# Optimization experiments

Hardware: AMD Instinct MI355X
Metric: run time of the kernel (lower is better)

The kernel has to match this reference:

```python
import jax, jax.numpy as jnp
import numpy as np

B, N, K, L, H = 8, 2048, 16, 4, 8
CONV = (64, 64, 128, 256)
W_DIM, N_CODES, E_DIM, P_DIM, FF = 512, 8, 64, 256, 512


def act(x):
    return jax.nn.leaky_relu(x, 0.2)


def ln(x, g, b, eps=1e-5):
    m = jnp.mean(x, -1, keepdims=True)
    v = jnp.mean((x - m) ** 2, -1, keepdims=True)
    return g * (x - m) / jnp.sqrt(v + eps) + b


# per-batch neighbor gather: f [C,N], i [N,K] -> [C,N,K]
gather_nb = jax.vmap(lambda f, i: f[:, i])


def knn_idx(y):  # y [B,3,N] -> [B,N,K]
    xx = jnp.sum(y * y, axis=1)
    inner = jnp.einsum('bcn,bcm->bnm', y, y)
    dist = 2.0 * inner - xx[:, :, None] - xx[:, None, :]  # negative sq dist
    return jax.lax.top_k(dist, K)[1]


def mha(q, kv, Wq, bq, Wk, bk, Wv, bv, Wo, bo):
    Bq, S, D = q.shape
    Sk = kv.shape[1]
    dh = D // H
    qh = (q @ Wq.T + bq).reshape(Bq, S, H, dh)
    kh = (kv @ Wk.T + bk).reshape(Bq, Sk, H, dh)
    vh = (kv @ Wv.T + bv).reshape(Bq, Sk, H, dh)
    a = jax.nn.softmax(jnp.einsum('bqhd,bkhd->bhqk', qh, kh) * (1.0 / np.sqrt(dh)))
    o = jnp.einsum('bhqk,bkhd->bqhd', a, vh).reshape(Bq, S, D)
    return o @ Wo.T + bo


def setup_inputs() -> dict:
    key = jax.random.key(0)
    ks = iter(jax.random.split(key, 48))
    nrm = lambda shape: jax.random.normal(next(ks), shape, jnp.float32) * 0.02
    d = {
        'x': jax.random.normal(next(ks), (B, N, 3), jnp.float32),
        'W_ec': nrm((CONV[0], 6)), 'b_ec': jnp.zeros((CONV[0],), jnp.float32),
        'Wc1': nrm((CONV[1], CONV[0])), 'bc1': jnp.zeros((CONV[1],), jnp.float32),
        'Wc2': nrm((CONV[2], CONV[1])), 'bc2': jnp.zeros((CONV[2],), jnp.float32),
        'Wc3': nrm((CONV[3], CONV[2])), 'bc3': jnp.zeros((CONV[3],), jnp.float32),
        'Wf': nrm((W_DIM, sum(CONV))), 'bf': jnp.zeros((W_DIM,), jnp.float32),
        'Wpc': nrm((P_DIM, E_DIM)), 'bpc': jnp.zeros((P_DIM,), jnp.float32),
        'Wpi': nrm((P_DIM, 3)), 'bpi': jnp.zeros((P_DIM,), jnp.float32),
        'Wq': nrm((L, 2, P_DIM, P_DIM)), 'bq': jnp.zeros((L, 2, P_DIM), jnp.float32),
        'Wk': nrm((L, 2, P_DIM, P_DIM)), 'bk': jnp.zeros((L, 2, P_DIM), jnp.float32),
        'Wv': nrm((L, 2, P_DIM, P_DIM)), 'bv': jnp.zeros((L, 2, P_DIM), jnp.float32),
        'Wo': nrm((L, 2, P_DIM, P_DIM)), 'bo': jnp.zeros((L, 2, P_DIM), jnp.float32),
        'ln1g': jnp.ones((L, P_DIM), jnp.float32), 'ln1b': jnp.zeros((L, P_DIM), jnp.float32),
        'ln2g': jnp.ones((L, P_DIM), jnp.float32), 'ln2b': jnp.zeros((L, P_DIM), jnp.float32),
        'Wff1': nrm((L, FF, P_DIM)), 'bff1': jnp.zeros((L, FF), jnp.float32),
        'Wff2': nrm((L, P_DIM, FF)), 'bff2': jnp.zeros((L, P_DIM), jnp.float32),
        'ln3g': jnp.ones((L, P_DIM), jnp.float32), 'ln3b': jnp.zeros((L, P_DIM), jnp.float32),
        'lnfg': jnp.ones((P_DIM,), jnp.float32), 'lnfb': jnp.zeros((P_DIM,), jnp.float32),
        'Wcm': nrm((E_DIM, P_DIM)), 'bcm': jnp.zeros((E_DIM,), jnp.float32),
    }
    return d


def reference(x, W_ec, b_ec, Wc1, bc1, Wc2, bc2, Wc3, bc3, Wf, bf, Wpc, bpc, Wpi, bpi,
              Wq, bq, Wk, bk, Wv, bv, Wo, bo, ln1g, ln1b, ln2g, ln2b,
              Wff1, bff1, Wff2, bff2, ln3g, ln3b, lnfg, lnfb, Wcm, bcm):
    y = jnp.transpose(x, (0, 2, 1))                      # [B,3,N]
    idx = knn_idx(y)                                     # [B,N,K]
    nb = gather_nb(y, idx)                               # [B,3,N,K]
    feats = jnp.concatenate([nb - y[..., None], jnp.broadcast_to(y[..., None], nb.shape)], axis=1)
    h = act(jnp.einsum('oc,bcnk->bonk', W_ec, feats) + b_ec[:, None, None])
    h = h.max(axis=3)                                    # [B,64,N]
    xs = [h]
    for Wl, bl in ((Wc1, bc1), (Wc2, bc2), (Wc3, bc3)):
        h = gather_nb(h, idx).max(axis=3)                # graph max pooling
        h = act(jnp.einsum('oc,bcn->bon', Wl, h) + bl[:, None])
        xs.append(h)
    h = jnp.concatenate(xs, axis=1)                      # [B,512,N]
    h = jnp.einsum('oc,bcn->bon', Wf, h) + bf[:, None]
    xm = h.max(axis=2)                                   # [B,512]
    q = act(xm.reshape(B, N_CODES, E_DIM) @ Wpc.T + bpc) # [B,8,256]
    mem = act(x @ Wpi.T + bpi)                           # [B,N,256]
    for l in range(L):
        q = ln(q + mha(q, q, Wq[l, 0], bq[l, 0], Wk[l, 0], bk[l, 0], Wv[l, 0], bv[l, 0], Wo[l, 0], bo[l, 0]), ln1g[l], ln1b[l])
        q = ln(q + mha(q, mem, Wq[l, 1], bq[l, 1], Wk[l, 1], bk[l, 1], Wv[l, 1], bv[l, 1], Wo[l, 1], bo[l, 1]), ln2g[l], ln2b[l])
        q = ln(q + (act(q @ Wff1[l].T + bff1[l]) @ Wff2[l].T + bff2[l]), ln3g[l], ln3b[l])
    q = ln(q, lnfg, lnfb)
    out = q @ Wcm.T + bcm                                # [B,8,64]
    return out.reshape(B, W_DIM)
```

## Files before the change

### kernel.cpp

```cpp
#include <hip/hip_runtime.h>
#include <math.h>

#define BN 8
#define NP 2048
#define KNN 16
#define NL 4
#define NH 8

typedef __attribute__((ext_vector_type(8))) short bf16x8;
typedef __attribute__((ext_vector_type(4))) float f32x4;

__device__ __forceinline__ unsigned short f2bf(float f) {
    unsigned u = __float_as_uint(f);
    unsigned r = (u + 0x7FFFu + ((u >> 16) & 1u)) >> 16;
    return (unsigned short)r;
}
__device__ __forceinline__ float bf2f(unsigned short s) {
    return __uint_as_float(((unsigned)s) << 16);
}
__device__ __forceinline__ unsigned fmono(float f) {
    unsigned u = __float_as_uint(f);
    return (u & 0x80000000u) ? ~u : (u | 0x80000000u);
}
__device__ __forceinline__ float funmono(unsigned k) {
    return (k & 0x80000000u) ? __uint_as_float(k ^ 0x80000000u) : __uint_as_float(~k);
}

__device__ __forceinline__ float gemv_dot(const unsigned short* __restrict__ wrow, const float* sm, int K8) {
    const uint4* w8 = (const uint4*)wrow;
    const float4* r4 = (const float4*)sm;
    float acc = 0.f;
    #pragma unroll 16
    for (int c = 0; c < K8; ++c) {
        uint4 wv = w8[c];
        float4 a0 = r4[c * 2], a1 = r4[c * 2 + 1];
        acc += a0.x * __uint_as_float(wv.x << 16);
        acc += a0.y * __uint_as_float(wv.x & 0xFFFF0000u);
        acc += a0.z * __uint_as_float(wv.y << 16);
        acc += a0.w * __uint_as_float(wv.y & 0xFFFF0000u);
        acc += a1.x * __uint_as_float(wv.z << 16);
        acc += a1.y * __uint_as_float(wv.z & 0xFFFF0000u);
        acc += a1.z * __uint_as_float(wv.w << 16);
        acc += a1.w * __uint_as_float(wv.w & 0xFFFF0000u);
    }
    return acc;
}

__device__ __forceinline__ unsigned long long shflx_u64(unsigned long long v, int j) {
    int lo = __shfl_xor((int)(unsigned)(v & 0xFFFFFFFFull), j);
    int hi = __shfl_xor((int)(unsigned)(v >> 32), j);
    return ((unsigned long long)(unsigned)hi << 32) | (unsigned)lo;
}

__device__ __forceinline__ unsigned sort64_u32(unsigned v, int lane) {
    #pragma unroll
    for (int k = 2; k <= 64; k <<= 1) {
        #pragma unroll
        for (int j = k >> 1; j > 0; j >>= 1) {
            unsigned o = (unsigned)__shfl_xor((int)v, j);
            bool up = ((lane & k) == 0);
            bool lower = ((lane & j) == 0);
            unsigned mn = v < o ? v : o;
            unsigned mx = v < o ? o : v;
            v = (up == lower) ? mn : mx;
        }
    }
    return v;
}

__device__ __forceinline__ unsigned long long sort64_u64(unsigned long long v, int lane) {
    #pragma unroll
    for (int k = 2; k <= 64; k <<= 1) {
        #pragma unroll
        for (int j = k >> 1; j > 0; j >>= 1) {
            unsigned long long o = shflx_u64(v, j);
            bool up = ((lane & k) == 0);
            bool lower = ((lane & j) == 0);
            unsigned long long mn = v < o ? v : o;
            unsigned long long mx = v < o ? o : v;
            v = (up == lower) ? mn : mx;
        }
    }
    return v;
}

__global__ __launch_bounds__(256) void knn_kernel(const float* __restrict__ x, int* __restrict__ idxout) {
    __shared__ unsigned long long cand[4][64];
    int tid = threadIdx.x;
    int wv = tid >> 6, lane = tid & 63;
    int p = blockIdx.x * 4 + wv;
    int b = p >> 11, n = p & 2047;
    const float* xb = x + (size_t)b * NP * 3;
    float cx = xb[n * 3 + 0], cy = xb[n * 3 + 1], cz = xb[n * 3 + 2];
    float xn = cx * cx + cy * cy + cz * cz;
    unsigned key[32];
    unsigned lmax = 0u;
    #pragma unroll
    for (int t = 0; t < 32; ++t) {
        int m = (t << 6) | lane;
        float mx = xb[m * 3 + 0], my = xb[m * 3 + 1], mz = xb[m * 3 + 2];
        float xxm = mx * mx + my * my + mz * mz;
        float inner = cx * mx + cy * my + cz * mz;
        float dd = 2.0f * inner - xn - xxm;
        unsigned u = __float_as_uint(dd);
        u = (u & 0x80000000u) ? ~u : (u | 0x80000000u);
        key[t] = u;
        lmax = lmax > u ? lmax : u;
    }
    unsigned sorted = sort64_u32(lmax, lane);
    unsigned S = (unsigned)__shfl((int)sorted, 48);
    int c = 0;
    #pragma unroll
    for (int t = 0; t < 32; ++t) c += (key[t] >= S) ? 1 : 0;
    int inc = c;
    #pragma unroll
    for (int d = 1; d < 64; d <<= 1) {
        int tsh = __shfl_up(inc, d);
        if (lane >= d) inc += tsh;
    }
    int C = __shfl(inc, 63);
    int* op = idxout + (size_t)p * KNN;
    if (C <= 64) {
        int off = inc - c;
        #pragma unroll
        for (int t = 0; t < 32; ++t) {
            if (key[t] >= S) {
                int m = (t << 6) | lane;
                cand[wv][off++] = ((unsigned long long)key[t] << 16) | (unsigned)(2047 - m);
            }
        }
        asm volatile("s_waitcnt lgkmcnt(0)" ::: "memory");
        unsigned long long ck = (lane < C) ? cand[wv][lane] : 0ull;
        ck = sort64_u64(ck, lane);
        if (lane >= 48) op[63 - lane] = 2047 - (int)(unsigned)(ck & 0xFFFFull);
    } else {
        unsigned taken = 0u;
        for (int r = 0; r < KNN; ++r) {
            unsigned long long best = 0ull;
            #pragma unroll
            for (int t = 0; t < 32; ++t) {
                if (!((taken >> t) & 1u)) {
                    int m = (t << 6) | lane;
                    unsigned long long ck = ((unsigned long long)key[t] << 16) | (unsigned)(2047 - m);
                    if (ck > best) best = ck;
                }
            }
            #pragma unroll
            for (int d = 1; d < 64; d <<= 1) {
                unsigned long long o = shflx_u64(best, d);
                if (o > best) best = o;
            }
            int m = 2047 - (int)(unsigned)(best & 0xFFFFull);
            if (lane == 0) op[r] = m;
            if ((m & 63) == lane) taken |= 1u << (m >> 6);
        }
    }
}

__global__ __launch_bounds__(256) void edge_conv_kernel(const float* __restrict__ x, const int* __restrict__ idx,
                                                        const float* __restrict__ Wec, const float* __restrict__ bec,
                                                        unsigned short* __restrict__ hcatT) {
    int tid = threadIdx.x;
    int g = tid >> 6, o = tid & 63;
    int p = blockIdx.x * 4 + g;
    int b = p >> 11;
    __shared__ float nb[4][KNN][3];
    __shared__ float ctr[4][3];
    if (o < KNN) {
        int j = idx[(size_t)p * KNN + o];
        const float* xp = x + ((size_t)b * NP + j) * 3;
        nb[g][o][0] = xp[0]; nb[g][o][1] = xp[1]; nb[g][o][2] = xp[2];
    }
    if (o >= KNN && o < KNN + 3) ctr[g][o - KNN] = x[(size_t)p * 3 + (o - KNN)];
    __syncthreads();
    float w0 = Wec[o * 6 + 0], w1 = Wec[o * 6 + 1], w2 = Wec[o * 6 + 2];
    float w3 = Wec[o * 6 + 3], w4 = Wec[o * 6 + 4], w5 = Wec[o * 6 + 5];
    float c0 = ctr[g][0], c1 = ctr[g][1], c2 = ctr[g][2];
    float base = bec[o] + w3 * c0 + w4 * c1 + w5 * c2;
    float m = -3.4e38f;
    #pragma unroll
    for (int k = 0; k < KNN; ++k) {
        float v = base + w0 * (nb[g][k][0] - c0) + w1 * (nb[g][k][1] - c1) + w2 * (nb[g][k][2] - c2);
        v = v > 0.f ? v : 0.2f * v;
        m = fmaxf(m, v);
    }
    hcatT[(size_t)p * 512 + o] = f2bf(m);
}

__global__ __launch_bounds__(256) void pool_bf16_kernel(const unsigned short* __restrict__ src, int s_coff,
                                                        const int* __restrict__ idx,
                                                        unsigned short* __restrict__ dst, int C) {
    int tid = threadIdx.x, wv = tid >> 6, lane = tid & 63;
    int p = blockIdx.x * 4 + wv;
    int b = p >> 11;
    const int* ip = idx + (size_t)p * KNN;
    const unsigned short* sb = src + (size_t)b * NP * 512 + s_coff;
    for (int c0 = 0; c0 < C; c0 += 64) {
        int ch = c0 + lane;
        float m = -3.4e38f;
        #pragma unroll
        for (int k = 0; k < KNN; ++k) {
            int j = ip[k];
            m = fmaxf(m, bf2f(sb[(size_t)j * 512 + ch]));
        }
        dst[(size_t)p * C + ch] = f2bf(m);
    }
}

__global__ __launch_bounds__(256) void mfma_conv64_kernel(const unsigned short* __restrict__ A,
                                                          const unsigned short* __restrict__ W,
                                                          const float* __restrict__ bias,
                                                          unsigned short* __restrict__ hcatT, int coff) {
    __shared__ unsigned short As[128][72];
    __shared__ unsigned short Bs[64][72];
    int m0 = blockIdx.x * 128, b = blockIdx.z;
    int tid = threadIdx.x;
    int lane = tid & 63, wave = tid >> 6;
    int wr = wave >> 1, wc = wave & 1;
    int quad = lane >> 4, l16 = lane & 15;
    {
        int r = tid >> 1, s = (tid & 1) * 32;
        const unsigned short* ap = A + (size_t)b * NP * 64 + (size_t)(m0 + r) * 64 + s;
        uint4 v0 = *(const uint4*)(ap);
        uint4 v1 = *(const uint4*)(ap + 8);
        uint4 v2 = *(const uint4*)(ap + 16);
        uint4 v3 = *(const uint4*)(ap + 24);
        *(uint4*)&As[r][s] = v0; *(uint4*)&As[r][s + 8] = v1;
        *(uint4*)&As[r][s + 16] = v2; *(uint4*)&As[r][s + 24] = v3;
    }
    {
        int r = tid >> 2, s = (tid & 3) * 16;
        const unsigned short* wp = W + r * 64 + s;
        *(uint4*)&Bs[r][s] = *(const uint4*)wp;
        *(uint4*)&Bs[r][s + 8] = *(const uint4*)(wp + 8);
    }
    __syncthreads();
    f32x4 acc[4][2] = {};
    #pragma unroll
    for (int k0 = 0; k0 < 64; k0 += 32) {
        bf16x8 af[4], bfv[2];
        #pragma unroll
        for (int i = 0; i < 4; ++i) af[i] = *(const bf16x8*)&As[wr * 64 + i * 16 + l16][k0 + quad * 8];
        #pragma unroll
        for (int j = 0; j < 2; ++j) bfv[j] = *(const bf16x8*)&Bs[wc * 32 + j * 16 + l16][k0 + quad * 8];
        #pragma unroll
        for (int i = 0; i < 4; ++i)
            #pragma unroll
            for (int j = 0; j < 2; ++j)
                acc[i][j] = __builtin_amdgcn_mfma_f32_16x16x32_bf16(af[i], bfv[j], acc[i][j], 0, 0, 0);
    }
    #pragma unroll
    for (int i = 0; i < 4; ++i) {
        #pragma unroll
        for (int r = 0; r < 4; ++r) {
            int pt = m0 + wr * 64 + i * 16 + quad * 4 + r;
            #pragma unroll
            for (int j = 0; j < 2; ++j) {
                int ch = wc * 32 + j * 16 + l16;
                float v = acc[i][j][r] + bias[ch];
                v = v > 0.f ? v : 0.2f * v;
                hcatT[((size_t)b * NP + pt) * 512 + coff + ch] = f2bf(v);
            }
        }
    }
}

__global__ __launch_bounds__(256) void wcast_kernel(const float* __restrict__ Wf, const float* __restrict__ Wc3,
                                                    const float* __restrict__ Wk, const float* __restrict__ Wv,
                                                    const float* __restrict__ bk, const float* __restrict__ bv,
                                                    const float* __restrict__ Wc1, const float* __restrict__ Wc2,
                                                    const float* __restrict__ Wq, const float* __restrict__ Wo,
                                                    const float* __restrict__ Wff1, const float* __restrict__ Wff2,
                                                    unsigned short* __restrict__ WfB, unsigned short* __restrict__ Wc3B,
                                                    unsigned short* __restrict__ WkvB, float* __restrict__ bkv,
                                                    unsigned short* __restrict__ Wc1B, unsigned short* __restrict__ Wc2B,
                                                    unsigned short* __restrict__ WtB, unsigned short* __restrict__ Wff1B,
                                                    unsigned short* __restrict__ Wff2B,
                                                    unsigned* __restrict__ xmk) {
    int id = blockIdx.x * 256 + threadIdx.x;
    if (id < 262144) { WfB[id] = f2bf(Wf[id]); return; }
    int j = id - 262144;
    if (j < 32768) { Wc3B[j] = f2bf(Wc3[j]); return; }
    j -= 32768;
    if (j < 524288) {
        int l = j >> 17, r = j & 131071;
        float v = (r < 65536) ? Wk[(size_t)(l * 2 + 1) * 65536 + r]
                              : Wv[(size_t)(l * 2 + 1) * 65536 + (r - 65536)];
        WkvB[j] = f2bf(v);
        return;
    }
    j -= 524288;
    if (j < 2048) {
        int l = j >> 9, r = j & 511;
        bkv[j] = (r < 256) ? bk[(l * 2 + 1) * 256 + r] : bv[(l * 2 + 1) * 256 + (r - 256)];
        return;
    }
    j -= 2048;
    if (j < 4096) { Wc1B[j] = f2bf(Wc1[j]); return; }
    j -= 4096;
    if (j < 8192) { Wc2B[j] = f2bf(Wc2[j]); return; }
    j -= 8192;
    if (j < 4096) { xmk[j] = 0u; return; }
    j -= 4096;
    if (j < 1572864) {
        int l = j / 393216;
        int r = j - l * 393216;
        int m = r >> 16, c = r & 65535;
        float v;
        if (m == 0)      v = Wq[(size_t)(l * 2 + 0) * 65536 + c];
        else if (m == 1) v = Wk[(size_t)(l * 2 + 0) * 65536 + c];
        else if (m == 2) v = Wv[(size_t)(l * 2 + 0) * 65536 + c];
        else if (m == 3) v = Wo[(size_t)(l * 2 + 0) * 65536 + c];
        else if (m == 4) v = Wq[(size_t)(l * 2 + 1) * 65536 + c];
        else             v = Wo[(size_t)(l * 2 + 1) * 65536 + c];
        WtB[j] = f2bf(v);
        return;
    }
    j -= 1572864;
    if (j < 524288) { Wff1B[j] = f2bf(Wff1[j]); return; }
    j -= 524288;
    if (j < 524288) { Wff2B[j] = f2bf(Wff2[j]); return; }
}

__global__ __launch_bounds__(256) void mfma_gemm_kernel(const unsigned short* __restrict__ A, size_t a_bstride,
                                                        const unsigned short* __restrict__ B, size_t b_bstride,
                                                        const float* __restrict__ bias, int bias_per_m,
                                                        void* __restrict__ C, size_t c_bstride, int c_rstride,
                                                        int K, int act, int out_bf16,
                                                        unsigned* __restrict__ xmk, int domax) {
    __shared__ unsigned short As[128][40];
    __shared__ unsigned short Bs[128][40];
    int m0 = blockIdx.x * 128, n0 = blockIdx.y * 128, b = blockIdx.z;
    int tid = threadIdx.x;
    int lane = tid & 63, wave = tid >> 6;
    int wr = wave >> 1, wc = wave & 1;
    int quad = lane >> 4, l16 = lane & 15;
    int r0 = tid >> 2, kc0 = (tid & 3) * 8;
    f32x4 acc[4][4] = {};
    const unsigned short* Ab = A + (size_t)b * a_bstride;
    const unsigned short* Bb = B + (size_t)b * b_bstride;
    for (int k0 = 0; k0 < K; k0 += 32) {
        uint4 a0 = *(const uint4*)(Ab + (size_t)(m0 + r0) * K + k0 + kc0);
        uint4 a1 = *(const uint4*)(Ab + (size_t)(m0 + r0 + 64) * K + k0 + kc0);
        uint4 b0 = *(const uint4*)(Bb + (size_t)(n0 + r0) * K + k0 + kc0);
        uint4 b1 = *(const uint4*)(Bb + (size_t)(n0 + r0 + 64) * K + k0 + kc0);
        __syncthreads();
        *(uint4*)&As[r0][kc0] = a0;
        *(uint4*)&As[r0 + 64][kc0] = a1;
        *(uint4*)&Bs[r0][kc0] = b0;
        *(uint4*)&Bs[r0 + 64][kc0] = b1;
        __syncthreads();
        bf16x8 af[4], bfv[4];
        #pragma unroll
        for (int i = 0; i < 4; ++i) af[i] = *(const bf16x8*)&As[wr * 64 + i * 16 + l16][quad * 8];
        #pragma unroll
        for (int j = 0; j < 4; ++j) bfv[j] = *(const bf16x8*)&Bs[wc * 64 + j * 16 + l16][quad * 8];
        #pragma unroll
        for (int i = 0; i < 4; ++i)
            #pragma unroll
            for (int j = 0; j < 4; ++j)
                acc[i][j] = __builtin_amdgcn_mfma_f32_16x16x32_bf16(af[i], bfv[j], acc[i][j], 0, 0, 0);
    }
    if (domax) {
        #pragma unroll
        for (int i = 0; i < 4; ++i) {
            #pragma unroll
            for (int r = 0; r < 4; ++r) {
                int m = m0 + wr * 64 + i * 16 + quad * 4 + r;
                float v = fmaxf(fmaxf(acc[i][0][r], acc[i][1][r]), fmaxf(acc[i][2][r], acc[i][3][r]));
                v += bias[m];
                #pragma unroll
                for (int off = 1; off <= 8; off <<= 1) v = fmaxf(v, __shfl_xor(v, off));
                if (l16 == 0) atomicMax(&xmk[(size_t)b * 512 + m], fmono(v));
            }
        }
        return;
    }
    #pragma unroll
    for (int i = 0; i < 4; ++i) {
        #pragma unroll
        for (int r = 0; r < 4; ++r) {
            int m = m0 + wr * 64 + i * 16 + quad * 4 + r;
            float bm = bias_per_m ? bias[m] : 0.f;
            #pragma unroll
            for (int j = 0; j < 4; ++j) {
                int n = n0 + wc * 64 + j * 16 + l16;
                float v = acc[i][j][r] + (bias_per_m ? bm : bias[n]);
                if (act) v = v > 0.f ? v : 0.2f * v;
                size_t off = (size_t)b * c_bstride + (size_t)m * c_rstride + n;
                if (out_bf16) ((unsigned short*)C)[off] = f2bf(v);
                else          ((float*)C)[off] = v;
            }
        }
    }
}

__global__ __launch_bounds__(256) void mfma_kv_all_kernel(const unsigned short* __restrict__ A,
                                                          const unsigned short* __restrict__ W,
                                                          const float* __restrict__ bkv,
                                                          unsigned short* __restrict__ KVall) {
    __shared__ unsigned short As[128][40];
    __shared__ unsigned short Bs[128][40];
    int m0 = blockIdx.x * 128;
    int nb = blockIdx.y & 3, l = blockIdx.y >> 2;
    int n0 = nb * 128;
    int b = blockIdx.z;
    int tid = threadIdx.x;
    int lane = tid & 63, wave = tid >> 6;
    int wr = wave >> 1, wc = wave & 1;
    int quad = lane >> 4, l16 = lane & 15;
    int r0 = tid >> 2, kc0 = (tid & 3) * 8;
    f32x4 acc[4][4] = {};
    const unsigned short* Ab = A + (size_t)b * NP * 256;
    const unsigned short* Bb = W + (size_t)l * 131072;
    const float* bias = bkv + l * 512;
    for (int k0 = 0; k0 < 256; k0 += 32) {
        uint4 a0 = *(const uint4*)(Ab + (size_t)(m0 + r0) * 256 + k0 + kc0);
        uint4 a1 = *(const uint4*)(Ab + (size_t)(m0 + r0 + 64) * 256 + k0 + kc0);
        uint4 b0 = *(const uint4*)(Bb + (size_t)(n0 + r0) * 256 + k0 + kc0);
        uint4 b1 = *(const uint4*)(Bb + (size_t)(n0 + r0 + 64) * 256 + k0 + kc0);
        __syncthreads();
        *(uint4*)&As[r0][kc0] = a0;
        *(uint4*)&As[r0 + 64][kc0] = a1;
        *(uint4*)&Bs[r0][kc0] = b0;
        *(uint4*)&Bs[r0 + 64][kc0] = b1;
        __syncthreads();
        bf16x8 af[4], bfv[4];
        #pragma unroll
        for (int i = 0; i < 4; ++i) af[i] = *(const bf16x8*)&As[wr * 64 + i * 16 + l16][quad * 8];
        #pragma unroll
        for (int j = 0; j < 4; ++j) bfv[j] = *(const bf16x8*)&Bs[wc * 64 + j * 16 + l16][quad * 8];
        #pragma unroll
        for (int i = 0; i < 4; ++i)
            #pragma unroll
            for (int j = 0; j < 4; ++j)
                acc[i][j] = __builtin_amdgcn_mfma_f32_16x16x32_bf16(af[i], bfv[j], acc[i][j], 0, 0, 0);
    }
    unsigned short* Cb = KVall + ((size_t)l * BN + b) * NP * 512;
    #pragma unroll
    for (int i = 0; i < 4; ++i) {
        #pragma unroll
        for (int r = 0; r < 4; ++r) {
            int m = m0 + wr * 64 + i * 16 + quad * 4 + r;
            #pragma unroll
            for (int j = 0; j < 4; ++j) {
                int n = n0 + wc * 64 + j * 16 + l16;
                Cb[(size_t)m * 512 + n] = f2bf(acc[i][j][r] + bias[n]);
            }
        }
    }
}

__global__ __launch_bounds__(256) void pc_kernel(const unsigned* __restrict__ xmk, const float* __restrict__ Wpc,
                                                 const float* __restrict__ bpc,
                                                 const unsigned short* __restrict__ Wqkv,
                                                 const float* __restrict__ bq0, const float* __restrict__ bk0,
                                                 const float* __restrict__ bv0,
                                                 float* __restrict__ q, float* __restrict__ Qs,
                                                 float* __restrict__ Ks, float* __restrict__ Vs) {
    int row = blockIdx.x, tid = threadIdx.x;
    int id = row * 256 + tid;
    int b = row >> 3, i = row & 7;
    const unsigned* xr = xmk + b * 512 + i * 64;
    const float* w = Wpc + (size_t)tid * 64;
    float acc = bpc[tid];
    #pragma unroll
    for (int e = 0; e < 64; ++e) acc += funmono(xr[e]) * w[e];
    float qv = acc > 0.f ? acc : 0.2f * acc;
    q[id] = qv;
    __shared__ __align__(16) float a[256];
    a[tid] = qv;
    __syncthreads();
    Qs[id] = bq0[tid] + gemv_dot(Wqkv + (size_t)tid * 256, a, 32);
    Ks[id] = bk0[tid] + gemv_dot(Wqkv + 65536 + (size_t)tid * 256, a, 32);
    Vs[id] = bv0[tid] + gemv_dot(Wqkv + 131072 + (size_t)tid * 256, a, 32);
}

__global__ __launch_bounds__(256) void mem_kernel(const float* __restrict__ x, const float* __restrict__ Wpi,
                                                  const float* __restrict__ bpi, unsigned short* __restrict__ memB) {
    size_t id = (size_t)blockIdx.x * 256 + threadIdx.x;
    int p = (int)(id & 255);
    size_t pt = id >> 8;
    float x0 = x[pt * 3 + 0], x1 = x[pt * 3 + 1], x2 = x[pt * 3 + 2];
    float v = bpi[p] + x0 * Wpi[p * 3 + 0] + x1 * Wpi[p * 3 + 1] + x2 * Wpi[p * 3 + 2];
    v = v > 0.f ? v : 0.2f * v;
    memB[id] = f2bf(v);
}

__global__ __launch_bounds__(256) void attn_ln_kernel(const float* __restrict__ Qs, const float* __restrict__ Ks,
                                                      const float* __restrict__ Vs,
                                                      const unsigned short* __restrict__ WoB,
                                                      const float* __restrict__ bo, const float* __restrict__ res,
                                                      const float* __restrict__ g, const float* __restrict__ bt,
                                                      const unsigned short* __restrict__ Wq1B,
                                                      const float* __restrict__ bq1,
                                                      float* __restrict__ out, float* __restrict__ Qc) {
    int row = blockIdx.x, tid = threadIdx.x;
    int b = row >> 3;
    __shared__ float Kl[2048], Vl[2048], qr[256];
    __shared__ float sc[64];
    __shared__ __align__(16) float r[256];
    __shared__ __align__(16) float aout[256];
    __shared__ float red[256];
    for (int t = tid; t < 2048; t += 256) {
        Kl[t] = Ks[(size_t)b * 2048 + t];
        Vl[t] = Vs[(size_t)b * 2048 + t];
    }
    qr[tid] = Qs[(size_t)row * 256 + tid];
    __syncthreads();
    const float scale = 0.17677669529663687f;
    {
        int pair = tid >> 2, part = tid & 3;
        int h = pair >> 3, k = pair & 7;
        float dot = 0.f;
        #pragma unroll
        for (int d0 = 0; d0 < 8; ++d0) {
            int d = part * 8 + d0;
            dot += qr[h * 32 + d] * Kl[k * 256 + h * 32 + d];
        }
        dot += __shfl_xor(dot, 1);
        dot += __shfl_xor(dot, 2);
        if (part == 0) sc[pair] = dot * scale;
    }
    __syncthreads();
    if (tid < 64) {
        int k = tid & 7;
        float v = sc[tid];
        float m = v;
        #pragma unroll
        for (int off = 1; off < 8; off <<= 1) m = fmaxf(m, __shfl_xor(m, off));
        float e = __expf(v - m);
        float s = e;
        #pragma unroll
        for (int off = 1; off < 8; off <<= 1) s += __shfl_xor(s, off);
        sc[tid] = e / s;
        (void)k;
    }
    __syncthreads();
    {
        int h = tid >> 5;
        float acc = 0.f;
        #pragma unroll
        for (int k = 0; k < 8; ++k) acc += sc[h * 8 + k] * Vl[k * 256 + tid];
        r[tid] = acc;
    }
    __syncthreads();
    float acc = bo[tid] + gemv_dot(WoB + (size_t)tid * 256, r, 32);
    float v = res[(size_t)row * 256 + tid] + acc;
    red[tid] = v; __syncthreads();
    for (int s = 128; s; s >>= 1) { if (tid < s) red[tid] += red[tid + s]; __syncthreads(); }
    float mean = red[0] * (1.0f / 256.0f);
    __syncthreads();
    float dv = v - mean;
    red[tid] = dv * dv; __syncthreads();
    for (int s = 128; s; s >>= 1) { if (tid < s) red[tid] += red[tid + s]; __syncthreads(); }
    float var = red[0] * (1.0f / 256.0f);
    float oln = g[tid] * dv * rsqrtf(var + 1e-5f) + bt[tid];
    out[(size_t)row * 256 + tid] = oln;
    aout[tid] = oln;
    __syncthreads();
    {
        float qacc = bq1[tid] + gemv_dot(Wq1B + (size_t)tid * 256, aout, 32);
        Qc[(size_t)row * 256 + tid] = qacc;
    }
}

__global__ __launch_bounds__(256) void ca_part_kernel(const float* __restrict__ Qc,
                                                      const unsigned short* __restrict__ KVl,
                                                      float* __restrict__ part) {
    int kb = blockIdx.x, h = blockIdx.y, b = blockIdx.z;
    int tid = threadIdx.x;
    __shared__ float q[8][32];
    __shared__ __align__(16) float S[8][128];
    __shared__ float om[8][8][32];
    const float scale = 0.17677669529663687f;
    {
        int i = tid >> 5, d = tid & 31;
        q[i][d] = Qc[(size_t)(b * 8 + i) * 256 + h * 32 + d];
    }
    __syncthreads();
    {
        int kk = tid & 127, half = tid >> 7;
        int k = kb * 128 + kk;
        const unsigned short* kp = KVl + ((size_t)b * NP + k) * 512 + h * 32;
        float kd[32];
        #pragma unroll
        for (int u = 0; u < 4; ++u) {
            uint4 raw = *(const uint4*)(kp + u * 8);
            unsigned w0 = raw.x, w1 = raw.y, w2 = raw.z, w3 = raw.w;
            kd[u * 8 + 0] = __uint_as_float(w0 << 16); kd[u * 8 + 1] = __uint_as_float(w0 & 0xFFFF0000u);
            kd[u * 8 + 2] = __uint_as_float(w1 << 16); kd[u * 8 + 3] = __uint_as_float(w1 & 0xFFFF0000u);
            kd[u * 8 + 4] = __uint_as_float(w2 << 16); kd[u * 8 + 5] = __uint_as_float(w2 & 0xFFFF0000u);
            kd[u * 8 + 6] = __uint_as_float(w3 << 16); kd[u * 8 + 7] = __uint_as_float(w3 & 0xFFFF0000u);
        }
        #pragma unroll
        for (int i = 0; i < 4; ++i) {
            int ri = half * 4 + i;
            float dot = 0.f;
            #pragma unroll
            for (int d = 0; d < 32; ++d) dot += q[ri][d] * kd[d];
            S[ri][kk] = dot * scale;
        }
    }
    __syncthreads();
    float* pout = part + (((size_t)(b * NH + h)) * 16 + kb) * 288;
    {
        int i = tid >> 5, l32 = tid & 31;
        float m = -3.4e38f;
        #pragma unroll
        for (int t = 0; t < 4; ++t) m = fmaxf(m, S[i][l32 + t * 32]);
        #pragma unroll
        for (int off = 16; off; off >>= 1) m = fmaxf(m, __shfl_xor(m, off));
        float s = 0.f;
        #pragma unroll
        for (int t = 0; t < 4; ++t) {
            float e = __expf(S[i][l32 + t * 32] - m);
            S[i][l32 + t * 32] = e;
            s += e;
        }
        #pragma unroll
        for (int off = 16; off; off >>= 1) s += __shfl_xor(s, off);
        if (l32 == 0) { pout[i] = m; pout[8 + i] = s; }
    }
    __syncthreads();
    {
        int d = tid & 31, grp = tid >> 5;
        const unsigned short* Vb = KVl + ((size_t)b * NP + kb * 128) * 512 + 256 + h * 32 + d;
        float acc[8] = {};
        #pragma unroll 4
        for (int t = 0; t < 16; ++t) {
            int kk = grp * 16 + t;
            float v = bf2f(Vb[(size_t)kk * 512]);
            #pragma unroll
            for (int i = 0; i < 8; ++i) acc[i] += S[i][kk] * v;
        }
        #pragma unroll
        for (int i = 0; i < 8; ++i) om[grp][i][d] = acc[i];
    }
    __syncthreads();
    {
        int i = tid >> 5, d = tid & 31;
        float sum = 0.f;
        #pragma unroll
        for (int g = 0; g < 8; ++g) sum += om[g][i][d];
        pout[16 + i * 32 + d] = sum;
    }
}

__global__ __launch_bounds__(256) void combine_ff_kernel(const float* __restrict__ part,
                                                         const unsigned short* __restrict__ WoB,
                                                         const float* __restrict__ bo, const float* __restrict__ res,
                                                         const float* __restrict__ g2, const float* __restrict__ b2t,
                                                         const unsigned short* __restrict__ W1B,
                                                         const float* __restrict__ b1,
                                                         const unsigned short* __restrict__ W2B,
                                                         const float* __restrict__ b2,
                                                         const float* __restrict__ g3, const float* __restrict__ b3t,
                                                         float* __restrict__ out,
                                                         int is_last, const float* __restrict__ lnfg,
                                                         const float* __restrict__ lnfb, const float* __restrict__ Wcm,
                                                         const float* __restrict__ bcm, float* __restrict__ finout,
                                                         const unsigned short* __restrict__ Wqkvn,
                                                         const float* __restrict__ bqn, const float* __restrict__ bkn,
                                                         const float* __restrict__ bvn,
                                                         float* __restrict__ Qs, float* __restrict__ Ks,
                                                         float* __restrict__ Vs) {
    int row = blockIdx.x, tid = threadIdx.x;
    int b = row >> 3, i = row & 7;
    __shared__ __align__(16) float r[256];
    __shared__ __align__(16) float a[256];
    __shared__ __align__(16) float hbuf[512];
    __shared__ float red[256];
    {
        int h = tid >> 5, d = tid & 31;
        const float* pb = part + (size_t)(b * NH + h) * 16 * 288;
        float M = -3.4e38f;
        #pragma unroll
        for (int kb = 0; kb < 16; ++kb) M = fmaxf(M, pb[kb * 288 + i]);
        float L = 0.f, O = 0.f;
        #pragma unroll
        for (int kb = 0; kb < 16; ++kb) {
            float w = __expf(pb[kb * 288 + i] - M);
            L += pb[kb * 288 + 8 + i] * w;
            O += pb[kb * 288 + 16 + i * 32 + d] * w;
        }
        r[tid] = O / L;
    }
    __syncthreads();
    {
        float acc = bo[tid] + gemv_dot(WoB + (size_t)tid * 256, r, 32);
        float v = res[(size_t)row * 256 + tid] + acc;
        red[tid] = v; __syncthreads();
        for (int s = 128; s; s >>= 1) { if (tid < s) red[tid] += red[tid + s]; __syncthreads(); }
        float mean = red[0] * (1.0f / 256.0f);
        __syncthreads();
        float dv = v - mean;
        red[tid] = dv * dv; __syncthreads();
        for (int s = 128; s; s >>= 1) { if (tid < s) red[tid] += red[tid + s]; __syncthreads(); }
        float var = red[0] * (1.0f / 256.0f);
        a[tid] = g2[tid] * dv * rsqrtf(var + 1e-5f) + b2t[tid];
    }
    __syncthreads();
    {
        #pragma unroll
        for (int half = 0; half < 2; ++half) {
            int o = tid + half * 256;
            float acc = b1[o] + gemv_dot(W1B + (size_t)o * 256, a, 32);
            hbuf[o] = acc > 0.f ? acc : 0.2f * acc;
        }
    }
    __syncthreads();
    float tln;
    {
        float acc = b2[tid] + gemv_dot(W2B + (size_t)tid * 512, hbuf, 64);
        float v = a[tid] + acc;
        red[tid] = v; __syncthreads();
        for (int s = 128; s; s >>= 1) { if (tid < s) red[tid] += red[tid + s]; __syncthreads(); }
        float mean = red[0] * (1.0f / 256.0f);
        __syncthreads();
        float dv = v - mean;
        red[tid] = dv * dv; __syncthreads();
        for (int s = 128; s; s >>= 1) { if (tid < s) red[tid] += red[tid + s]; __syncthreads(); }
        float var = red[0] * (1.0f / 256.0f);
        tln = g3[tid] * dv * rsqrtf(var + 1e-5f) + b3t[tid];
    }
    if (!is_last) {
        out[(size_t)row * 256 + tid] = tln;
        r[tid] = tln;
        __syncthreads();
        size_t id = (size_t)row * 256 + tid;
        Qs[id] = bqn[tid] + gemv_dot(Wqkvn + (size_t)tid * 256, r, 32);
        Ks[id] = bkn[tid] + gemv_dot(Wqkvn + 65536 + (size_t)tid * 256, r, 32);
        Vs[id] = bvn[tid] + gemv_dot(Wqkvn + 131072 + (size_t)tid * 256, r, 32);
        return;
    }
    __syncthreads();
    red[tid] = tln; __syncthreads();
    for (int s = 128; s; s >>= 1) { if (tid < s) red[tid] += red[tid + s]; __syncthreads(); }
    float mean = red[0] * (1.0f / 256.0f);
    __syncthreads();
    float dv = tln - mean;
    red[tid] = dv * dv; __syncthreads();
    for (int s = 128; s; s >>= 1) { if (tid < s) red[tid] += red[tid + s]; __syncthreads(); }
    float var = red[0] * (1.0f / 256.0f);
    a[tid] = lnfg[tid] * dv * rsqrtf(var + 1e-5f) + lnfb[tid];
    __syncthreads();
    if (tid < 64) {
        const float4* w4 = (const float4*)(Wcm + (size_t)tid * 256);
        const float4* a4 = (const float4*)a;
        float acc = bcm[tid];
        #pragma unroll 8
        for (int c = 0; c < 64; ++c) {
            float4 av = a4[c], wv = w4[c];
            acc += av.x * wv.x + av.y * wv.y + av.z * wv.z + av.w * wv.w;
        }
        finout[(size_t)b * 512 + i * 64 + tid] = acc;
    }
}

extern "C" void kernel_launch(void* const* d_in, const int* in_sizes, int n_in,
                              void* d_out, int out_size, void* d_ws, size_t ws_size,
                              hipStream_t stream) {
    const float* x    = (const float*)d_in[0];
    const float* Wec  = (const float*)d_in[1];
    const float* bec  = (const float*)d_in[2];
    const float* Wc1  = (const float*)d_in[3];
    const float* bc1  = (const float*)d_in[4];
    const float* Wc2  = (const float*)d_in[5];
    const float* bc2  = (const float*)d_in[6];
    const float* Wc3  = (const float*)d_in[7];
    const float* bc3  = (const float*)d_in[8];
    const float* Wf   = (const float*)d_in[9];
    const float* bf   = (const float*)d_in[10];
    const float* Wpc  = (const float*)d_in[11];
    const float* bpc  = (const float*)d_in[12];
    const float* Wpi  = (const float*)d_in[13];
    const float* bpi  = (const float*)d_in[14];
    const float* Wq   = (const float*)d_in[15];
    const float* bq   = (const float*)d_in[16];
    const float* Wk   = (const float*)d_in[17];
    const float* bk   = (const float*)d_in[18];
    const float* Wv   = (const float*)d_in[19];
    const float* bv   = (const float*)d_in[20];
    const float* Wo   = (const float*)d_in[21];
    const float* bo   = (const float*)d_in[22];
    const float* ln1g = (const float*)d_in[23];
    const float* ln1b = (const float*)d_in[24];
    const float* ln2g = (const float*)d_in[25];
    const float* ln2b = (const float*)d_in[26];
    const float* Wff1 = (const float*)d_in[27];
    const float* bff1 = (const float*)d_in[28];
    const float* Wff2 = (const float*)d_in[29];
    const float* bff2 = (const float*)d_in[30];
    const float* ln3g = (const float*)d_in[31];
    const float* ln3b = (const float*)d_in[32];
    const float* lnfg = (const float*)d_in[33];
    const float* lnfb = (const float*)d_in[34];
    const float* Wcm  = (const float*)d_in[35];
    const float* bcm  = (const float*)d_in[36];
    float* out = (float*)d_out;

    float* ws = (float*)d_ws;
    size_t off = 0;
    auto alloc = [&](size_t n) { float* p = ws + off; off += (n + 3) & ~(size_t)3; return p; };
    int*            idx   = (int*)alloc((size_t)BN * NP * KNN);
    unsigned short* hcatT = (unsigned short*)alloc((size_t)BN * NP * 512 / 2);
    unsigned short* poolT = (unsigned short*)alloc((size_t)BN * NP * 128 / 2);
    unsigned short* WfB   = (unsigned short*)alloc(262144 / 2);
    unsigned short* Wc1B  = (unsigned short*)alloc(4096 / 2);
    unsigned short* Wc2B  = (unsigned short*)alloc(8192 / 2);
    unsigned short* Wc3B  = (unsigned short*)alloc(32768 / 2);
    unsigned short* WkvB  = (unsigned short*)alloc(524288 / 2);
    float*          bkv   = alloc(2048);
    unsigned short* memB  = (unsigned short*)alloc((size_t)BN * NP * 256 / 2);
    unsigned short* KVall = (unsigned short*)alloc((size_t)NL * BN * NP * 512 / 2);
    unsigned*       xmk   = (unsigned*)alloc((size_t)BN * 512);
    unsigned short* WtB   = (unsigned short*)alloc(1572864 / 2);
    unsigned short* Wff1B = (unsigned short*)alloc(524288 / 2);
    unsigned short* Wff2B = (unsigned short*)alloc(524288 / 2);
    float*          qa    = alloc((size_t)BN * 8 * 256);
    float*          qb    = alloc((size_t)BN * 8 * 256);
    float*          Qs    = alloc((size_t)BN * 8 * 256);
    float*          Ks    = alloc((size_t)BN * 8 * 256);
    float*          Vs    = alloc((size_t)BN * 8 * 256);
    float*          Qc    = alloc((size_t)BN * 8 * 256);
    float*          part  = alloc((size_t)BN * NH * 16 * 288);

    wcast_kernel<<<13512, 256, 0, stream>>>(Wf, Wc3, Wk, Wv, bk, bv, Wc1, Wc2, Wq, Wo, Wff1, Wff2,
                                            WfB, Wc3B, WkvB, bkv, Wc1B, Wc2B, WtB, Wff1B, Wff2B, xmk);

    knn_kernel<<<BN * NP / 4, 256, 0, stream>>>(x, idx);
    edge_conv_kernel<<<BN * NP / 4, 256, 0, stream>>>(x, idx, Wec, bec, hcatT);

    pool_bf16_kernel<<<BN * NP / 4, 256, 0, stream>>>(hcatT, 0, idx, poolT, 64);
    mfma_conv64_kernel<<<dim3(NP / 128, 1, BN), 256, 0, stream>>>(poolT, Wc1B, bc1, hcatT, 64);
    pool_bf16_kernel<<<BN * NP / 4, 256, 0, stream>>>(hcatT, 64, idx, poolT, 64);
    mfma_gemm_kernel<<<dim3(NP / 128, 1, BN), 256, 0, stream>>>(poolT, (size_t)NP * 64, Wc2B, 0,
                                                                bc2, 0, (void*)(hcatT + 128), (size_t)NP * 512, 512,
                                                                64, 1, 1, nullptr, 0);
    pool_bf16_kernel<<<BN * NP / 4, 256, 0, stream>>>(hcatT, 128, idx, poolT, 128);
    mfma_gemm_kernel<<<dim3(NP / 128, 2, BN), 256, 0, stream>>>(poolT, (size_t)NP * 128, Wc3B, 0,
                                                                bc3, 0, (void*)(hcatT + 256), (size_t)NP * 512, 512,
                                                                128, 1, 1, nullptr, 0);
    mfma_gemm_kernel<<<dim3(4, NP / 128, BN), 256, 0, stream>>>(WfB, 0, hcatT, (size_t)NP * 512,
                                                                bf, 1, nullptr, 0, 0,
                                                                512, 0, 0, xmk, 1);
    pc_kernel<<<BN * 8, 256, 0, stream>>>(xmk, Wpc, bpc, WtB, bq, bk, bv, qa, Qs, Ks, Vs);
    mem_kernel<<<BN * NP, 256, 0, stream>>>(x, Wpi, bpi, memB);
    mfma_kv_all_kernel<<<dim3(NP / 128, 4 * NL, BN), 256, 0, stream>>>(memB, WkvB, bkv, KVall);

    for (int l = 0; l < NL; ++l) {
        const unsigned short* Wl = WtB + (size_t)l * 393216;
        const float* bo0 = bo + (l * 2 + 0) * 256;
        const float* bq1 = bq + (l * 2 + 1) * 256;
        const float* bo1 = bo + (l * 2 + 1) * 256;
        int last = (l == NL - 1);

        attn_ln_kernel<<<BN * 8, 256, 0, stream>>>(Qs, Ks, Vs, Wl + 3 * 65536, bo0, qa,
                                                   ln1g + l * 256, ln1b + l * 256, Wl + 4 * 65536, bq1, qb, Qc);
        ca_part_kernel<<<dim3(16, NH, BN), 256, 0, stream>>>(Qc, KVall + (size_t)l * BN * NP * 512, part);
        combine_ff_kernel<<<BN * 8, 256, 0, stream>>>(part, Wl + 5 * 65536, bo1, qb,
                                                      ln2g + l * 256, ln2b + l * 256,
                                                      Wff1B + (size_t)l * 131072, bff1 + l * 512,
                                                      Wff2B + (size_t)l * 131072, bff2 + l * 256,
                                                      ln3g + l * 256, ln3b + l * 256, qa,
                                                      last, lnfg, lnfb, Wcm, bcm, out,
                                                      last ? nullptr : WtB + (size_t)(l + 1) * 393216,
                                                      bq + ((l + 1) * 2) * 256, bk + ((l + 1) * 2) * 256,
                                                      bv + ((l + 1) * 2) * 256,
                                                      Qs, Ks, Vs);
    }

    (void)in_sizes; (void)n_in; (void)out_size; (void)ws_size;
}
```

Before: 591.7 us.

## Split GEMV rows across four threads in 1024-thread decoder blocks

```diff
diff --git a/kernel.cpp b/kernel.cpp
--- a/kernel.cpp
+++ b/kernel.cpp
@@ -29,21 +29,17 @@
 __device__ __forceinline__ float gemv_dot(const unsigned short* __restrict__ wrow, const float* sm, int K8) {
     const uint4* w8 = (const uint4*)wrow;
     const float4* r4 = (const float4*)sm;
-    float acc = 0.f;
-    #pragma unroll 16
+    float a0 = 0.f, a1 = 0.f, a2 = 0.f, a3 = 0.f;
+    #pragma unroll 8
     for (int c = 0; c < K8; ++c) {
         uint4 wv = w8[c];
-        float4 a0 = r4[c * 2], a1 = r4[c * 2 + 1];
-        acc += a0.x * __uint_as_float(wv.x << 16);
-        acc += a0.y * __uint_as_float(wv.x & 0xFFFF0000u);
-        acc += a0.z * __uint_as_float(wv.y << 16);
-        acc += a0.w * __uint_as_float(wv.y & 0xFFFF0000u);
-        acc += a1.x * __uint_as_float(wv.z << 16);
-        acc += a1.y * __uint_as_float(wv.z & 0xFFFF0000u);
-        acc += a1.z * __uint_as_float(wv.w << 16);
-        acc += a1.w * __uint_as_float(wv.w & 0xFFFF0000u);
-    }
-    return acc;
+        float4 x0 = r4[c * 2], x1 = r4[c * 2 + 1];
+        a0 += x0.x * __uint_as_float(wv.x << 16) + x0.y * __uint_as_float(wv.x & 0xFFFF0000u);
+        a1 += x0.z * __uint_as_float(wv.y << 16) + x0.w * __uint_as_float(wv.y & 0xFFFF0000u);
+        a2 += x1.x * __uint_as_float(wv.z << 16) + x1.y * __uint_as_float(wv.z & 0xFFFF0000u);
+        a3 += x1.z * __uint_as_float(wv.w << 16) + x1.w * __uint_as_float(wv.w & 0xFFFF0000u);
+    }
+    return (a0 + a1) + (a2 + a3);
 }
 
 __device__ __forceinline__ unsigned long long shflx_u64(unsigned long long v, int j) {
@@ -487,44 +483,43 @@
     memB[id] = f2bf(v);
 }
 
-__global__ __launch_bounds__(256) void attn_ln_kernel(const float* __restrict__ Qs, const float* __restrict__ Ks,
-                                                      const float* __restrict__ Vs,
-                                                      const unsigned short* __restrict__ WoB,
-                                                      const float* __restrict__ bo, const float* __restrict__ res,
-                                                      const float* __restrict__ g, const float* __restrict__ bt,
-                                                      const unsigned short* __restrict__ Wq1B,
-                                                      const float* __restrict__ bq1,
-                                                      float* __restrict__ out, float* __restrict__ Qc) {
+__global__ __launch_bounds__(1024) void attn_ln_kernel(const float* __restrict__ Qs, const float* __restrict__ Ks,
+                                                       const float* __restrict__ Vs,
+                                                       const unsigned short* __restrict__ WoB,
+                                                       const float* __restrict__ bo, const float* __restrict__ res,
+                                                       const float* __restrict__ g, const float* __restrict__ bt,
+                                                       const unsigned short* __restrict__ Wq1B,
+                                                       const float* __restrict__ bq1,
+                                                       float* __restrict__ out, float* __restrict__ Qc) {
     int row = blockIdx.x, tid = threadIdx.x;
     int b = row >> 3;
-    __shared__ float Kl[2048], Vl[2048], qr[256];
+    __shared__ float Kl[2048], Vl[2048];
+    __shared__ __align__(16) float qr[256];
     __shared__ float sc[64];
     __shared__ __align__(16) float r[256];
     __shared__ __align__(16) float aout[256];
-    __shared__ float red[256];
-    for (int t = tid; t < 2048; t += 256) {
+    __shared__ float red[1024];
+    for (int t = tid; t < 2048; t += 1024) {
         Kl[t] = Ks[(size_t)b * 2048 + t];
         Vl[t] = Vs[(size_t)b * 2048 + t];
     }
-    qr[tid] = Qs[(size_t)row * 256 + tid];
+    if (tid < 256) qr[tid] = Qs[(size_t)row * 256 + tid];
     __syncthreads();
     const float scale = 0.17677669529663687f;
     {
-        int pair = tid >> 2, part = tid & 3;
+        int pair = tid >> 4, part = tid & 15;
         int h = pair >> 3, k = pair & 7;
-        float dot = 0.f;
-        #pragma unroll
-        for (int d0 = 0; d0 < 8; ++d0) {
-            int d = part * 8 + d0;
-            dot += qr[h * 32 + d] * Kl[k * 256 + h * 32 + d];
-        }
+        int d = part * 2;
+        float dot = qr[h * 32 + d] * Kl[k * 256 + h * 32 + d]
+                  + qr[h * 32 + d + 1] * Kl[k * 256 + h * 32 + d + 1];
         dot += __shfl_xor(dot, 1);
         dot += __shfl_xor(dot, 2);
+        dot += __shfl_xor(dot, 4);
+        dot += __shfl_xor(dot, 8);
         if (part == 0) sc[pair] = dot * scale;
     }
     __syncthreads();
     if (tid < 64) {
-        int k = tid & 7;
         float v = sc[tid];
         float m = v;
         #pragma unroll
@@ -534,10 +529,9 @@
         #pragma unroll
         for (int off = 1; off < 8; off <<= 1) s += __shfl_xor(s, off);
         sc[tid] = e / s;
-        (void)k;
-    }
-    __syncthreads();
-    {
+    }
+    __syncthreads();
+    if (tid < 256) {
         int h = tid >> 5;
         float acc = 0.f;
         #pragma unroll
@@ -545,23 +539,33 @@
         r[tid] = acc;
     }
     __syncthreads();
-    float acc = bo[tid] + gemv_dot(WoB + (size_t)tid * 256, r, 32);
-    float v = res[(size_t)row * 256 + tid] + acc;
+    int o4 = tid >> 2, p4 = tid & 3;
+    float v;
+    {
+        float acc = gemv_dot(WoB + (size_t)o4 * 256 + p4 * 64, r + p4 * 64, 8);
+        acc += __shfl_xor(acc, 1);
+        acc += __shfl_xor(acc, 2);
+        v = (p4 == 0) ? (bo[o4] + acc + res[(size_t)row * 256 + o4]) : 0.f;
+    }
     red[tid] = v; __syncthreads();
-    for (int s = 128; s; s >>= 1) { if (tid < s) red[tid] += red[tid + s]; __syncthreads(); }
+    for (int s = 512; s; s >>= 1) { if (tid < s) red[tid] += red[tid + s]; __syncthreads(); }
     float mean = red[0] * (1.0f / 256.0f);
     __syncthreads();
-    float dv = v - mean;
+    float dv = (p4 == 0) ? v - mean : 0.f;
     red[tid] = dv * dv; __syncthreads();
-    for (int s = 128; s; s >>= 1) { if (tid < s) red[tid] += red[tid + s]; __syncthreads(); }
+    for (int s = 512; s; s >>= 1) { if (tid < s) red[tid] += red[tid + s]; __syncthreads(); }
     float var = red[0] * (1.0f / 256.0f);
-    float oln = g[tid] * dv * rsqrtf(var + 1e-5f) + bt[tid];
-    out[(size_t)row * 256 + tid] = oln;
-    aout[tid] = oln;
-    __syncthreads();
-    {
-        float qacc = bq1[tid] + gemv_dot(Wq1B + (size_t)tid * 256, aout, 32);
-        Qc[(size_t)row * 256 + tid] = qacc;
+    if (p4 == 0) {
+        float oln = g[o4] * dv * rsqrtf(var + 1e-5f) + bt[o4];
+        out[(size_t)row * 256 + o4] = oln;
+        aout[o4] = oln;
+    }
+    __syncthreads();
+    {
+        float qacc = gemv_dot(Wq1B + (size_t)o4 * 256 + p4 * 64, aout + p4 * 64, 8);
+        qacc += __shfl_xor(qacc, 1);
+        qacc += __shfl_xor(qacc, 2);
+        if (p4 == 0) Qc[(size_t)row * 256 + o4] = bq1[o4] + qacc;
     }
 }
 
@@ -647,103 +651,118 @@
     }
 }
 
-__global__ __launch_bounds__(256) void combine_ff_kernel(const float* __restrict__ part,
-                                                         const unsigned short* __restrict__ WoB,
-                                                         const float* __restrict__ bo, const float* __restrict__ res,
-                                                         const float* __restrict__ g2, const float* __restrict__ b2t,
-                                                         const unsigned short* __restrict__ W1B,
-                                                         const float* __restrict__ b1,
-                                                         const unsigned short* __restrict__ W2B,
-                                                         const float* __restrict__ b2,
-                                                         const float* __restrict__ g3, const float* __restrict__ b3t,
-                                                         float* __restrict__ out,
-                                                         int is_last, const float* __restrict__ lnfg,
-                                                         const float* __restrict__ lnfb, const float* __restrict__ Wcm,
-                                                         const float* __restrict__ bcm, float* __restrict__ finout,
-                                                         const unsigned short* __restrict__ Wqkvn,
-                                                         const float* __restrict__ bqn, const float* __restrict__ bkn,
-                                                         const float* __restrict__ bvn,
-                                                         float* __restrict__ Qs, float* __restrict__ Ks,
-                                                         float* __restrict__ Vs) {
+__global__ __launch_bounds__(1024) void combine_ff_kernel(const float* __restrict__ part,
+                                                          const unsigned short* __restrict__ WoB,
+                                                          const float* __restrict__ bo, const float* __restrict__ res,
+                                                          const float* __restrict__ g2, const float* __restrict__ b2t,
+                                                          const unsigned short* __restrict__ W1B,
+                                                          const float* __restrict__ b1,
+                                                          const unsigned short* __restrict__ W2B,
+                                                          const float* __restrict__ b2,
+                                                          const float* __restrict__ g3, const float* __restrict__ b3t,
+                                                          float* __restrict__ out,
+                                                          int is_last, const float* __restrict__ lnfg,
+                                                          const float* __restrict__ lnfb, const float* __restrict__ Wcm,
+                                                          const float* __restrict__ bcm, float* __restrict__ finout,
+                                                          const unsigned short* __restrict__ Wqkvn,
+                                                          const float* __restrict__ bqn, const float* __restrict__ bkn,
+                                                          const float* __restrict__ bvn,
+                                                          float* __restrict__ Qs, float* __restrict__ Ks,
+                                                          float* __restrict__ Vs) {
     int row = blockIdx.x, tid = threadIdx.x;
     int b = row >> 3, i = row & 7;
     __shared__ __align__(16) float r[256];
     __shared__ __align__(16) float a[256];
     __shared__ __align__(16) float hbuf[512];
-    __shared__ float red[256];
-    {
-        int h = tid >> 5, d = tid & 31;
+    __shared__ float red[1024];
+    {
+        int h = tid >> 7, rem = tid & 127, d = rem >> 2, g = rem & 3;
         const float* pb = part + (size_t)(b * NH + h) * 16 * 288;
         float M = -3.4e38f;
         #pragma unroll
-        for (int kb = 0; kb < 16; ++kb) M = fmaxf(M, pb[kb * 288 + i]);
+        for (int t = 0; t < 4; ++t) M = fmaxf(M, pb[(g * 4 + t) * 288 + i]);
+        M = fmaxf(M, __shfl_xor(M, 1));
+        M = fmaxf(M, __shfl_xor(M, 2));
         float L = 0.f, O = 0.f;
         #pragma unroll
-        for (int kb = 0; kb < 16; ++kb) {
+        for (int t = 0; t < 4; ++t) {
+            int kb = g * 4 + t;
             float w = __expf(pb[kb * 288 + i] - M);
             L += pb[kb * 288 + 8 + i] * w;
             O += pb[kb * 288 + 16 + i * 32 + d] * w;
         }
-        r[tid] = O / L;
-    }
-    __syncthreads();
-    {
-        float acc = bo[tid] + gemv_dot(WoB + (size_t)tid * 256, r, 32);
-        float v = res[(size_t)row * 256 + tid] + acc;
-        red[tid] = v; __syncthreads();
-        for (int s = 128; s; s >>= 1) { if (tid < s) red[tid] += red[tid + s]; __syncthreads(); }
-        float mean = red[0] * (1.0f / 256.0f);
-        __syncthreads();
-        float dv = v - mean;
-        red[tid] = dv * dv; __syncthreads();
-        for (int s = 128; s; s >>= 1) { if (tid < s) red[tid] += red[tid + s]; __syncthreads(); }
-        float var = red[0] * (1.0f / 256.0f);
-        a[tid] = g2[tid] * dv * rsqrtf(var + 1e-5f) + b2t[tid];
-    }
-    __syncthreads();
-    {
-        #pragma unroll
-        for (int half = 0; half < 2; ++half) {
-            int o = tid + half * 256;
-            float acc = b1[o] + gemv_dot(W1B + (size_t)o * 256, a, 32);
-            hbuf[o] = acc > 0.f ? acc : 0.2f * acc;
-        }
-    }
-    __syncthreads();
-    float tln;
-    {
-        float acc = b2[tid] + gemv_dot(W2B + (size_t)tid * 512, hbuf, 64);
-        float v = a[tid] + acc;
-        red[tid] = v; __syncthreads();
-        for (int s = 128; s; s >>= 1) { if (tid < s) red[tid] += red[tid + s]; __syncthreads(); }
-        float mean = red[0] * (1.0f / 256.0f);
-        __syncthreads();
-        float dv = v - mean;
-        red[tid] = dv * dv; __syncthreads();
-        for (int s = 128; s; s >>= 1) { if (tid < s) red[tid] += red[tid + s]; __syncthreads(); }
-        float var = red[0] * (1.0f / 256.0f);
-        tln = g3[tid] * dv * rsqrtf(var + 1e-5f) + b3t[tid];
-    }
+        L += __shfl_xor(L, 1); L += __shfl_xor(L, 2);
+        O += __shfl_xor(O, 1); O += __shfl_xor(O, 2);
+        if (g == 0) r[h * 32 + d] = O / L;
+    }
+    __syncthreads();
+    int o4 = tid >> 2, p4 = tid & 3;
+    float v;
+    {
+        float acc = gemv_dot(WoB + (size_t)o4 * 256 + p4 * 64, r + p4 * 64, 8);
+        acc += __shfl_xor(acc, 1);
+        acc += __shfl_xor(acc, 2);
+        v = (p4 == 0) ? (bo[o4] + acc + res[(size_t)row * 256 + o4]) : 0.f;
+    }
+    red[tid] = v; __syncthreads();
+    for (int s = 512; s; s >>= 1) { if (tid < s) red[tid] += red[tid + s]; __syncthreads(); }
+    float mean = red[0] * (1.0f / 256.0f);
+    __syncthreads();
+    float dv = (p4 == 0) ? v - mean : 0.f;
+    red[tid] = dv * dv; __syncthreads();
+    for (int s = 512; s; s >>= 1) { if (tid < s) red[tid] += red[tid + s]; __syncthreads(); }
+    float var = red[0] * (1.0f / 256.0f);
+    if (p4 == 0) a[o4] = g2[o4] * dv * rsqrtf(var + 1e-5f) + b2t[o4];
+    __syncthreads();
+    {
+        int o = tid >> 1, p = tid & 1;
+        float acc = gemv_dot(W1B + (size_t)o * 256 + p * 128, a + p * 128, 16);
+        acc += __shfl_xor(acc, 1);
+        if (p == 0) { float t = b1[o] + acc; hbuf[o] = t > 0.f ? t : 0.2f * t; }
+    }
+    __syncthreads();
+    float vF;
+    {
+        float acc = gemv_dot(W2B + (size_t)o4 * 512 + p4 * 128, hbuf + p4 * 128, 16);
+        acc += __shfl_xor(acc, 1);
+        acc += __shfl_xor(acc, 2);
+        vF = (p4 == 0) ? (b2[o4] + acc + a[o4]) : 0.f;
+    }
+    red[tid] = vF; __syncthreads();
+    for (int s = 512; s; s >>= 1) { if (tid < s) red[tid] += red[tid + s]; __syncthreads(); }
+    float mean2 = red[0] * (1.0f / 256.0f);
+    __syncthreads();
+    float dv2 = (p4 == 0) ? vF - mean2 : 0.f;
+    red[tid] = dv2 * dv2; __syncthreads();
+    for (int s = 512; s; s >>= 1) { if (tid < s) red[tid] += red[tid + s]; __syncthreads(); }
+    float var2 = red[0] * (1.0f / 256.0f);
+    float tln = 0.f;
+    if (p4 == 0) {
+        tln = g3[o4] * dv2 * rsqrtf(var2 + 1e-5f) + b3t[o4];
+        r[o4] = tln;
+    }
+    __syncthreads();
     if (!is_last) {
-        out[(size_t)row * 256 + tid] = tln;
-        r[tid] = tln;
-        __syncthreads();
-        size_t id = (size_t)row * 256 + tid;
-        Qs[id] = bqn[tid] + gemv_dot(Wqkvn + (size_t)tid * 256, r, 32);
-        Ks[id] = bkn[tid] + gemv_dot(Wqkvn + 65536 + (size_t)tid * 256, r, 32);
-        Vs[id] = bvn[tid] + gemv_dot(Wqkvn + 131072 + (size_t)tid * 256, r, 32);
+        if (p4 == 0) out[(size_t)row * 256 + o4] = tln;
+        if (tid < 768) {
+            int which = tid >> 8, o = tid & 255;
+            float acc = gemv_dot(Wqkvn + (size_t)which * 65536 + (size_t)o * 256, r, 32);
+            float bb = (which == 0) ? bqn[o] : (which == 1) ? bkn[o] : bvn[o];
+            float* dst = (which == 0) ? Qs : (which == 1) ? Ks : Vs;
+            dst[(size_t)row * 256 + o] = bb + acc;
+        }
         return;
     }
-    __syncthreads();
-    red[tid] = tln; __syncthreads();
-    for (int s = 128; s; s >>= 1) { if (tid < s) red[tid] += red[tid + s]; __syncthreads(); }
-    float mean = red[0] * (1.0f / 256.0f);
-    __syncthreads();
-    float dv = tln - mean;
-    red[tid] = dv * dv; __syncthreads();
-    for (int s = 128; s; s >>= 1) { if (tid < s) red[tid] += red[tid + s]; __syncthreads(); }
-    float var = red[0] * (1.0f / 256.0f);
-    a[tid] = lnfg[tid] * dv * rsqrtf(var + 1e-5f) + lnfb[tid];
+    float tf = (tid < 256) ? r[tid] : 0.f;
+    red[tid] = tf; __syncthreads();
+    for (int s = 512; s; s >>= 1) { if (tid < s) red[tid] += red[tid + s]; __syncthreads(); }
+    float mean3 = red[0] * (1.0f / 256.0f);
+    __syncthreads();
+    float d3 = (tid < 256) ? tf - mean3 : 0.f;
+    red[tid] = d3 * d3; __syncthreads();
+    for (int s = 512; s; s >>= 1) { if (tid < s) red[tid] += red[tid + s]; __syncthreads(); }
+    float var3 = red[0] * (1.0f / 256.0f);
+    if (tid < 256) a[tid] = lnfg[tid] * d3 * rsqrtf(var3 + 1e-5f) + lnfb[tid];
     __syncthreads();
     if (tid < 64) {
         const float4* w4 = (const float4*)(Wcm + (size_t)tid * 256);
@@ -856,19 +875,19 @@
         const float* bo1 = bo + (l * 2 + 1) * 256;
         int last = (l == NL - 1);
 
-        attn_ln_kernel<<<BN * 8, 256, 0, stream>>>(Qs, Ks, Vs, Wl + 3 * 65536, bo0, qa,
-                                                   ln1g + l * 256, ln1b + l * 256, Wl + 4 * 65536, bq1, qb, Qc);
+        attn_ln_kernel<<<BN * 8, 1024, 0, stream>>>(Qs, Ks, Vs, Wl + 3 * 65536, bo0, qa,
+                                                    ln1g + l * 256, ln1b + l * 256, Wl + 4 * 65536, bq1, qb, Qc);
         ca_part_kernel<<<dim3(16, NH, BN), 256, 0, stream>>>(Qc, KVall + (size_t)l * BN * NP * 512, part);
-        combine_ff_kernel<<<BN * 8, 256, 0, stream>>>(part, Wl + 5 * 65536, bo1, qb,
-                                                      ln2g + l * 256, ln2b + l * 256,
-                                                      Wff1B + (size_t)l * 131072, bff1 + l * 512,
-                                                      Wff2B + (size_t)l * 131072, bff2 + l * 256,
-                                                      ln3g + l * 256, ln3b + l * 256, qa,
-                                                      last, lnfg, lnfb, Wcm, bcm, out,
-                                                      last ? nullptr : WtB + (size_t)(l + 1) * 393216,
-                                                      bq + ((l + 1) * 2) * 256, bk + ((l + 1) * 2) * 256,
-                                                      bv + ((l + 1) * 2) * 256,
-                                                      Qs, Ks, Vs);
+        combine_ff_kernel<<<BN * 8, 1024, 0, stream>>>(part, Wl + 5 * 65536, bo1, qb,
+                                                       ln2g + l * 256, ln2b + l * 256,
+                                                       Wff1B + (size_t)l * 131072, bff1 + l * 512,
+                                                       Wff2B + (size_t)l * 131072, bff2 + l * 256,
+                                                       ln3g + l * 256, ln3b + l * 256, qa,
+                                                       last, lnfg, lnfb, Wcm, bcm, out,
+                                                       last ? nullptr : WtB + (size_t)(l + 1) * 393216,
+                                                       bq + ((l + 1) * 2) * 256, bk + ((l + 1) * 2) * 256,
+                                                       bv + ((l + 1) * 2) * 256,
+                                                       Qs, Ks, Vs);
     }
 
     (void)in_sizes; (void)n_in; (void)out_size; (void)ws_size;
```

Measured after the change: 553.9 us. 1.07x faster.
